# Kernel tuning notes

Measured on AMD Instinct MI355X. Metric: run time of the kernel, lower is better.

The kernel has to match this reference:

```python
import jax, jax.numpy as jnp
import numpy as np
from jax import lax

B, N, C_IN = 8, 4096, 64
NPOINT, NSAMPLE, RADIUS = 1024, 32, 0.2
BN_EPS = 1e-3  # keras BatchNormalization default epsilon


def _fps(pts):
    """Farthest point sampling on a single cloud pts: (N, 3) -> (NPOINT,) int32."""
    n = pts.shape[0]
    def step(carry, _):
        dist, far = carry
        c = pts[far]                                  # (3,)
        d = jnp.sum((pts - c) ** 2, axis=-1)          # (N,)
        dist = jnp.minimum(dist, d)
        nxt = jnp.argmax(dist).astype(jnp.int32)
        return (dist, nxt), far
    init = (jnp.full((n,), 1e10, pts.dtype), jnp.array(0, jnp.int32))
    _, idx = lax.scan(step, init, None, length=NPOINT)
    return idx


def _ball_query(xyz, new_xyz):
    """xyz: (B,N,3), new_xyz: (B,P,3) -> idx (B,P,NSAMPLE) int32.
    First NSAMPLE point indices within RADIUS of each centroid (in original
    order); slots beyond the in-ball count are filled with the first in-ball
    index, matching the PointNet++ CUDA query_ball_point semantics."""
    n = xyz.shape[1]
    # squared distances via the expansion trick to avoid a (B,P,N,3) temp
    d2 = (jnp.sum(new_xyz ** 2, -1)[:, :, None]
          + jnp.sum(xyz ** 2, -1)[:, None, :]
          - 2.0 * jnp.einsum('bpc,bnc->bpn', new_xyz, xyz))  # (B,P,N)
    in_ball = d2 < RADIUS ** 2
    cand = jnp.where(in_ball, jnp.arange(n, dtype=jnp.int32)[None, None, :], n)
    neg_top, _ = lax.top_k(-cand, NSAMPLE)   # NSAMPLE smallest indices
    idx = -neg_top                           # ascending order
    first = idx[..., :1]                     # centroid itself is always in-ball
    idx = jnp.where(idx == n, first, idx)
    return idx


def _group(feats, idx):
    """feats: (B,N,C), idx: (B,P,S) -> (B,P,S,C) gather per batch."""
    return jax.vmap(lambda f, i: f[i])(feats, idx)


def _mlp_layer(x, W, g, b, m, v):
    # 1x1 conv (no bias) + BN (inference stats) + ReLU
    x = jnp.einsum('bpsc,cd->bpsd', x, W)
    x = (x - m) * lax.rsqrt(v + BN_EPS) * g + b
    return jax.nn.relu(x)


def setup_inputs() -> dict:
    key = jax.random.key(0)
    ks = jax.random.split(key, 8)
    xyz = jax.random.uniform(ks[0], (B, N, 3), dtype=jnp.float32)
    points = jax.random.normal(ks[1], (B, N, C_IN), dtype=jnp.float32)
    c0 = 3 + C_IN  # use_xyz=True
    W0 = jax.random.normal(ks[2], (c0, 64), jnp.float32) / np.sqrt(c0)
    W1 = jax.random.normal(ks[3], (64, 64), jnp.float32) / np.sqrt(64.0)
    W2 = jax.random.normal(ks[4], (64, 128), jnp.float32) / np.sqrt(64.0)
    def bn(c):
        return (jnp.ones((c,), jnp.float32), jnp.zeros((c,), jnp.float32),
                jnp.zeros((c,), jnp.float32), jnp.ones((c,), jnp.float32))
    g0, b0, m0, v0 = bn(64)
    g1, b1, m1, v1 = bn(64)
    g2, b2, m2, v2 = bn(128)
    return dict(xyz=xyz, points=points,
                W0=W0, g0=g0, b0=b0, m0=m0, v0=v0,
                W1=W1, g1=g1, b1=b1, m1=m1, v1=v1,
                W2=W2, g2=g2, b2=b2, m2=m2, v2=v2)


def reference(xyz, points,
              W0, g0, b0, m0, v0,
              W1, g1, b1, m1, v1,
              W2, g2, b2, m2, v2):
    # --- sample_and_group ---
    fps_idx = jax.vmap(_fps)(xyz)                            # (B,P)
    new_xyz = jnp.take_along_axis(xyz, fps_idx[:, :, None], axis=1)  # (B,P,3)
    idx = _ball_query(xyz, new_xyz)                          # (B,P,S)
    grouped_xyz = _group(xyz, idx) - new_xyz[:, :, None, :]  # (B,P,S,3)
    grouped_pts = _group(points, idx)                        # (B,P,S,C)
    new_points = jnp.concatenate([grouped_xyz, grouped_pts], axis=-1)
    # --- shared per-point MLP (1x1 conv + BN + ReLU) ---
    new_points = _mlp_layer(new_points, W0, g0, b0, m0, v0)
    new_points = _mlp_layer(new_points, W1, g1, b1, m1, v1)
    new_points = _mlp_layer(new_points, W2, g2, b2, m2, v2)
    # --- max pool over the neighborhood axis ---
    new_points = jnp.max(new_points, axis=2)                 # (B,P,128)
    return new_xyz, new_points, idx
```

## Files before the change

kernel.cpp:

```cpp
#include <hip/hip_runtime.h>
#include <stdint.h>

#define BN_EPS 0.001f

typedef float v2f __attribute__((ext_vector_type(2)));


struct FpsSh {
  float px[4096], py[4096], pz[4096];
  unsigned long long wk[2][4];
  int curh[32];
};

struct WrkSh {
  float W0s[67 * 64];
  float W1s[64 * 64];
  float sh[64 * 36];
  float h0T[64 * 34];
  float s0c[64], t0c[64], s1c[64], t1c[64], s2c[128], t2c[128];
  float idxs[4 * 32];
  float cent[4 * 3];
};

union AllSh {
  FpsSh f;
  WrkSh w;
};

__global__ __launch_bounds__(256) void fused_kernel(
    const float* __restrict__ xyz, const float* __restrict__ points,
    const float* __restrict__ W0, const float* __restrict__ g0,
    const float* __restrict__ b0, const float* __restrict__ m0,
    const float* __restrict__ v0, const float* __restrict__ W1,
    const float* __restrict__ g1, const float* __restrict__ b1,
    const float* __restrict__ m1, const float* __restrict__ v1,
    const float* __restrict__ W2, const float* __restrict__ g2,
    const float* __restrict__ b2, const float* __restrict__ m2,
    const float* __restrict__ v2, float* __restrict__ new_xyz,
    float* __restrict__ new_points, float* __restrict__ idxf,
    unsigned int* __restrict__ prog) {
  __shared__ __align__(16) AllSh smem;
  const int bid = blockIdx.x;
  const int t = threadIdx.x;

  if (bid < 8) {
#pragma clang fp contract(off)
    float* px = smem.f.px;
    float* py = smem.f.py;
    float* pz = smem.f.pz;
    int* curh = smem.f.curh;
    auto& wk = smem.f.wk;
    const int lane = t & 63, wid = t >> 6;
    const int b = bid;
    const float* X = xyz + (size_t)b * 4096 * 3;
    float* out = new_xyz + (size_t)b * 1024 * 3;
    v2f x[8], y[8], z[8], dist[8];
#pragma unroll
    for (int j = 0; j < 8; ++j) {
      const int n0 = (2 * j) * 256 + t;
      const int n1 = (2 * j + 1) * 256 + t;
      x[j].x = X[n0 * 3 + 0]; x[j].y = X[n1 * 3 + 0];
      y[j].x = X[n0 * 3 + 1]; y[j].y = X[n1 * 3 + 1];
      z[j].x = X[n0 * 3 + 2]; z[j].y = X[n1 * 3 + 2];
      px[n0] = x[j].x; py[n0] = y[j].x; pz[n0] = z[j].x;
      px[n1] = x[j].y; py[n1] = y[j].y; pz[n1] = z[j].y;
      dist[j] = (v2f){1e10f, 1e10f};
    }
    __syncthreads();
    int cur = 0;
    for (int cc = 0; cc < 32; ++cc) {
      for (int ii = 0; ii < 32; ++ii) {
        const int it = cc * 32 + ii;
        if (t == 0) curh[ii] = cur;
        const float cx = px[cur], cy = py[cur], cz = pz[cur];
        const v2f cxv = {cx, cx}, cyv = {cy, cy}, czv = {cz, cz};
        float bestv = -1.0f;
        int bestj = 0;
#pragma unroll
        for (int j = 0; j < 8; ++j) {
          v2f dx = x[j] - cxv, dy = y[j] - cyv, dz = z[j] - czv;
          v2f d = dx * dx + dy * dy;
          d = d + dz * dz;
          v2f nd = __builtin_elementwise_min(dist[j], d);
          dist[j] = nd;
          if (nd.x > bestv) { bestv = nd.x; bestj = 2 * j; }
          if (nd.y > bestv) { bestv = nd.y; bestj = 2 * j + 1; }
        }
        const int besti = bestj * 256 + t;
        unsigned long long key =
            ((unsigned long long)__float_as_uint(bestv) << 32) | (unsigned)(~besti);
#define DPP_STEP(CTRL)                                                                     \
        {                                                                                  \
          unsigned lo_ = (unsigned)key, hi_ = (unsigned)(key >> 32);                       \
          unsigned ls = (unsigned)__builtin_amdgcn_update_dpp((int)lo_, (int)lo_, CTRL, 0xf, 0xf, false); \
          unsigned hs = (unsigned)__builtin_amdgcn_update_dpp((int)hi_, (int)hi_, CTRL, 0xf, 0xf, false); \
          unsigned long long sk = ((unsigned long long)hs << 32) | ls;                     \
          if (sk > key) key = sk;                                                          \
        }
        DPP_STEP(0x111)
        DPP_STEP(0x112)
        DPP_STEP(0x114)
        DPP_STEP(0x118)
        DPP_STEP(0x142)
        DPP_STEP(0x143)
#undef DPP_STEP
        const unsigned whi = (unsigned)__builtin_amdgcn_readlane((int)(key >> 32), 63);
        const unsigned wlo = (unsigned)__builtin_amdgcn_readlane((int)key, 63);
        if (lane == 0) wk[it & 1][wid] = ((unsigned long long)whi << 32) | wlo;
        __syncthreads();
        const unsigned long long k0 = wk[it & 1][0], k1 = wk[it & 1][1];
        const unsigned long long k2 = wk[it & 1][2], k3 = wk[it & 1][3];
        unsigned long long b01 = (k1 > k0) ? k1 : k0;
        unsigned long long b23 = (k3 > k2) ? k3 : k2;
        unsigned long long bk = (b23 > b01) ? b23 : b01;
        cur = (int)(~(unsigned)(bk & 0xffffffffull));
      }
      if (t == 0) {
        asm volatile("s_waitcnt vmcnt(0)" ::: "memory");
        if (cc > 0)
          __hip_atomic_store(&prog[b * 32], (unsigned)(cc * 32),
                             __ATOMIC_RELAXED, __HIP_MEMORY_SCOPE_AGENT);
      }
      if (t < 32) {
        const int c = curh[t];
        const int p = cc * 32 + t;
        __hip_atomic_store(&out[p * 3 + 0], px[c], __ATOMIC_RELAXED,
                           __HIP_MEMORY_SCOPE_AGENT);
        __hip_atomic_store(&out[p * 3 + 1], py[c], __ATOMIC_RELAXED,
                           __HIP_MEMORY_SCOPE_AGENT);
        __hip_atomic_store(&out[p * 3 + 2], pz[c], __ATOMIC_RELAXED,
                           __HIP_MEMORY_SCOPE_AGENT);
      }
      if (cc == 30 && t == 0) {
        asm volatile("s_waitcnt vmcnt(0)" ::: "memory");
        __hip_atomic_store(&prog[b * 32], 992u, __ATOMIC_RELAXED,
                           __HIP_MEMORY_SCOPE_AGENT);
      }
    }
    if (t == 0) {
      asm volatile("s_waitcnt vmcnt(0)" ::: "memory");
      __hip_atomic_store(&prog[b * 32], 1024u, __ATOMIC_RELAXED,
                         __HIP_MEMORY_SCOPE_AGENT);
    }
    return;
  }

  float* W0s = smem.w.W0s;
  float* W1s = smem.w.W1s;
  float* s0c = smem.w.s0c; float* t0c = smem.w.t0c;
  float* s1c = smem.w.s1c; float* t1c = smem.w.t1c;
  float* s2c = smem.w.s2c; float* t2c = smem.w.t2c;
  for (int i = t; i < 67 * 64; i += 256) W0s[i] = W0[i];
  for (int i = t; i < 64 * 64; i += 256) W1s[i] = W1[i];
  if (t < 64) {
    float s = g0[t] * rsqrtf(v0[t] + BN_EPS); s0c[t] = s; t0c[t] = b0[t] - m0[t] * s;
    float u = g1[t] * rsqrtf(v1[t] + BN_EPS); s1c[t] = u; t1c[t] = b1[t] - m1[t] * u;
  }
  if (t < 128) {
    float s = g2[t] * rsqrtf(v2[t] + BN_EPS); s2c[t] = s; t2c[t] = b2[t] - m2[t] * s;
  }
  __syncthreads();
  const int sgrp = t & 15, dgrp = t >> 4;
  const int dg2 = t & 31, sg2 = t >> 5;
  float* inT = smem.w.sh;
  float* h1T = smem.w.sh;
  float* h0T = smem.w.h0T;
  float* pmax = h0T;

  auto wait_prog = [&](int b, unsigned need) {
    int guard = 0;
    while (__hip_atomic_load(&prog[b * 32], __ATOMIC_RELAXED,
                             __HIP_MEMORY_SCOPE_AGENT) < need) {
      __builtin_amdgcn_s_sleep(8);
      if (++guard > (1 << 20)) break;
    }
  };

  auto process_group = [&](int b, int p0, int nc) {
    {
#pragma clang fp contract(off)
      const int wv = t >> 6, lane = t & 63;
      if (wv < nc) {
        const int pg = b * 1024 + p0 + wv;
        const float* X = xyz + (size_t)b * 4096 * 3;
        const float cx = __hip_atomic_load(&new_xyz[pg * 3 + 0], __ATOMIC_RELAXED,
                                           __HIP_MEMORY_SCOPE_AGENT);
        const float cy = __hip_atomic_load(&new_xyz[pg * 3 + 1], __ATOMIC_RELAXED,
                                           __HIP_MEMORY_SCOPE_AGENT);
        const float cz = __hip_atomic_load(&new_xyz[pg * 3 + 2], __ATOMIC_RELAXED,
                                           __HIP_MEMORY_SCOPE_AGENT);
        const float csq = (cx * cx + cy * cy) + cz * cz;
        float* outg = idxf + (size_t)pg * 32;
        float* ol = smem.w.idxs + wv * 32;
        int total = 0;
        int first = -1;
        float xx = X[lane * 3 + 0], yy = X[lane * 3 + 1], zz = X[lane * 3 + 2];
        for (int chunk = 0; chunk < 64; ++chunk) {
          const int n = chunk * 64 + lane;
          float nx = xx, ny = yy, nz = zz;
          if (chunk < 63) {
            const float* Xn = X + (n + 64) * 3;
            nx = Xn[0]; ny = Xn[1]; nz = Xn[2];
          }
          const float sq = (xx * xx + yy * yy) + zz * zz;
          const float dot = fmaf(cz, zz, fmaf(cy, yy, cx * xx));
          const float d2 = (csq + sq) - 2.0f * dot;
          const bool in = d2 < 0.04f;
          const unsigned long long mask = __ballot(in);
          if (first < 0 && mask != 0ull) first = chunk * 64 + __builtin_ctzll(mask);
          if (in) {
            const int pos = total + __builtin_popcountll(mask & ((1ull << lane) - 1ull));
            if (pos < 32) { outg[pos] = (float)n; ol[pos] = (float)n; }
          }
          total += __builtin_popcountll(mask);
          if (total >= 32) break;
          xx = nx; yy = ny; zz = nz;
        }
        if (total < 32 && first >= 0) {
          const int slot = total + lane;
          if (slot < 32) { outg[slot] = (float)first; ol[slot] = (float)first; }
        }
        if (lane == 0) {
          smem.w.cent[wv * 3 + 0] = cx;
          smem.w.cent[wv * 3 + 1] = cy;
          smem.w.cent[wv * 3 + 2] = cz;
        }
      }
    }
    __syncthreads();
    for (int pp = 0; pp < nc; ++pp) {
      const int pg = b * 1024 + p0 + pp;
      const float cx = smem.w.cent[pp * 3 + 0];
      const float cy = smem.w.cent[pp * 3 + 1];
      const float cz = smem.w.cent[pp * 3 + 2];
      {
        const int s = t >> 3, cg = t & 7;
        const int i = (int)smem.w.idxs[pp * 32 + s];
        const float* Pr = points + ((size_t)b * 4096 + i) * 64 + cg * 8;
        const float4 a = *(const float4*)Pr;
        const float4 c4 = *(const float4*)(Pr + 4);
        const int r = 3 + cg * 8;
        inT[(r + 0) * 34 + s] = a.x;  inT[(r + 1) * 34 + s] = a.y;
        inT[(r + 2) * 34 + s] = a.z;  inT[(r + 3) * 34 + s] = a.w;
        inT[(r + 4) * 34 + s] = c4.x; inT[(r + 5) * 34 + s] = c4.y;
        inT[(r + 6) * 34 + s] = c4.z; inT[(r + 7) * 34 + s] = c4.w;
        if (t < 32) {
          const int i2 = (int)smem.w.idxs[pp * 32 + t];
          const float* Xr = xyz + ((size_t)b * 4096 + i2) * 3;
          inT[0 * 34 + t] = Xr[0] - cx;
          inT[1 * 34 + t] = Xr[1] - cy;
          inT[2 * 34 + t] = Xr[2] - cz;
        }
      }
      __syncthreads();
      {
        float acc[2][4] = {{0, 0, 0, 0}, {0, 0, 0, 0}};
#pragma unroll 4
        for (int c = 0; c < 67; ++c) {
          const float2 a = *(const float2*)&inT[c * 34 + 2 * sgrp];
          const float4 w = *(const float4*)&W0s[c * 64 + 4 * dgrp];
          acc[0][0] = fmaf(a.x, w.x, acc[0][0]); acc[0][1] = fmaf(a.x, w.y, acc[0][1]);
          acc[0][2] = fmaf(a.x, w.z, acc[0][2]); acc[0][3] = fmaf(a.x, w.w, acc[0][3]);
          acc[1][0] = fmaf(a.y, w.x, acc[1][0]); acc[1][1] = fmaf(a.y, w.y, acc[1][1]);
          acc[1][2] = fmaf(a.y, w.z, acc[1][2]); acc[1][3] = fmaf(a.y, w.w, acc[1][3]);
        }
#pragma unroll
        for (int dj = 0; dj < 4; ++dj) {
          const int d = 4 * dgrp + dj;
          const float s = s0c[d], bb = t0c[d];
#pragma unroll
          for (int si = 0; si < 2; ++si) {
            float yv = fmaf(acc[si][dj], s, bb);
            h0T[d * 34 + 2 * sgrp + si] = fmaxf(yv, 0.0f);
          }
        }
      }
      __syncthreads();
      {
        float acc[2][4] = {{0, 0, 0, 0}, {0, 0, 0, 0}};
#pragma unroll 4
        for (int c = 0; c < 64; ++c) {
          const float2 a = *(const float2*)&h0T[c * 34 + 2 * sgrp];
          const float4 w = *(const float4*)&W1s[c * 64 + 4 * dgrp];
          acc[0][0] = fmaf(a.x, w.x, acc[0][0]); acc[0][1] = fmaf(a.x, w.y, acc[0][1]);
          acc[0][2] = fmaf(a.x, w.z, acc[0][2]); acc[0][3] = fmaf(a.x, w.w, acc[0][3]);
          acc[1][0] = fmaf(a.y, w.x, acc[1][0]); acc[1][1] = fmaf(a.y, w.y, acc[1][1]);
          acc[1][2] = fmaf(a.y, w.z, acc[1][2]); acc[1][3] = fmaf(a.y, w.w, acc[1][3]);
        }
#pragma unroll
        for (int dj = 0; dj < 4; ++dj) {
          const int d = 4 * dgrp + dj;
          const float s = s1c[d], bb = t1c[d];
#pragma unroll
          for (int si = 0; si < 2; ++si) {
            float yv = fmaf(acc[si][dj], s, bb);
            h1T[d * 36 + 2 * sgrp + si] = fmaxf(yv, 0.0f);
          }
        }
      }
      __syncthreads();
      {
        float acc[4][4] = {{0,0,0,0},{0,0,0,0},{0,0,0,0},{0,0,0,0}};
#pragma unroll 8
        for (int c = 0; c < 64; ++c) {
          const float4 a = *(const float4*)&h1T[c * 36 + 4 * sg2];
          const float4 w = *(const float4*)(W2 + c * 128 + 4 * dg2);
          acc[0][0] = fmaf(a.x, w.x, acc[0][0]); acc[0][1] = fmaf(a.x, w.y, acc[0][1]);
          acc[0][2] = fmaf(a.x, w.z, acc[0][2]); acc[0][3] = fmaf(a.x, w.w, acc[0][3]);
          acc[1][0] = fmaf(a.y, w.x, acc[1][0]); acc[1][1] = fmaf(a.y, w.y, acc[1][1]);
          acc[1][2] = fmaf(a.y, w.z, acc[1][2]); acc[1][3] = fmaf(a.y, w.w, acc[1][3]);
          acc[2][0] = fmaf(a.z, w.x, acc[2][0]); acc[2][1] = fmaf(a.z, w.y, acc[2][1]);
          acc[2][2] = fmaf(a.z, w.z, acc[2][2]); acc[2][3] = fmaf(a.z, w.w, acc[2][3]);
          acc[3][0] = fmaf(a.w, w.x, acc[3][0]); acc[3][1] = fmaf(a.w, w.y, acc[3][1]);
          acc[3][2] = fmaf(a.w, w.z, acc[3][2]); acc[3][3] = fmaf(a.w, w.w, acc[3][3]);
        }
#pragma unroll
        for (int dj = 0; dj < 4; ++dj) {
          const int d = 4 * dg2 + dj;
          const float s = s2c[d], bb = t2c[d];
          float mx = 0.0f;
#pragma unroll
          for (int si = 0; si < 4; ++si) {
            float yv = fmaf(acc[si][dj], s, bb);
            mx = fmaxf(mx, fmaxf(yv, 0.0f));
          }
          pmax[sg2 * 128 + d] = mx;
        }
      }
      __syncthreads();
      if (t < 128) {
        float mx = pmax[t];
#pragma unroll
        for (int g = 1; g < 8; ++g) mx = fmaxf(mx, pmax[g * 128 + t]);
        new_points[(size_t)pg * 128 + t] = mx;
      }
      __syncthreads();
    }
  };

  if (bid >= 256) {
    const int sid = bid - 256;
    const int b = sid & 7;
    const int q = sid >> 3;
    wait_prog(b, (unsigned)(960 + q + 1));
    process_group(b, 960 + q, 1);
    wait_prog(b, (unsigned)(992 + q + 1));
    process_group(b, 992 + q, 1);
  } else {
    for (int k = bid - 8; k < 1920; k += 248) {
      const int j = k >> 3, b = k & 7;
      wait_prog(b, (unsigned)(j * 4 + 4));
      process_group(b, j * 4, 4);
    }
  }
}

extern "C" void kernel_launch(void* const* d_in, const int* in_sizes, int n_in,
                              void* d_out, int out_size, void* d_ws, size_t ws_size,
                              hipStream_t stream) {
  (void)in_sizes; (void)n_in; (void)out_size; (void)ws_size;
  const float* xyz    = (const float*)d_in[0];
  const float* points = (const float*)d_in[1];
  const float* W0 = (const float*)d_in[2];
  const float* g0 = (const float*)d_in[3];
  const float* b0 = (const float*)d_in[4];
  const float* m0 = (const float*)d_in[5];
  const float* v0 = (const float*)d_in[6];
  const float* W1 = (const float*)d_in[7];
  const float* g1 = (const float*)d_in[8];
  const float* b1 = (const float*)d_in[9];
  const float* m1 = (const float*)d_in[10];
  const float* v1 = (const float*)d_in[11];
  const float* W2 = (const float*)d_in[12];
  const float* g2 = (const float*)d_in[13];
  const float* b2 = (const float*)d_in[14];
  const float* m2 = (const float*)d_in[15];
  const float* v2 = (const float*)d_in[16];

  float* new_xyz    = (float*)d_out;
  float* new_points = new_xyz + 8 * 1024 * 3;
  float* idxf       = new_points + 8 * 1024 * 128;

  unsigned int* prog = (unsigned int*)d_ws;
  hipMemsetAsync(d_ws, 0, 8 * 32 * sizeof(unsigned int), stream);
  fused_kernel<<<512, 256, 0, stream>>>(xyz, points, W0, g0, b0, m0, v0,
                                        W1, g1, b1, m1, v1,
                                        W2, g2, b2, m2, v2,
                                        new_xyz, new_points, idxf, prog);
}
```

Before: 699.8 us.

## Split FPS and worker shared memory, adaptive spin sleep, rebalance tail groups

The FPS and worker shared-memory layouts now sit in two separate arrays instead of one union, so every block reserves both (about 49KB plus 41KB). This lowers the number of blocks that fit per CU. The spin-wait sleeps longer when the producer is far behind, to cut polling traffic while FPS runs. Points 960-991 move from the single-point tail blocks into the 4-point group loop, so tail blocks only handle the last 32 points. This changes how consumers overlap with the sequential FPS producer but may reduce occupancy.

Measured after the change: 709.3 us. No clear change (+1.3%).

```diff
diff --git a/kernel.cpp b/kernel.cpp
--- a/kernel.cpp
+++ b/kernel.cpp
@@ -20,11 +20,6 @@
   float s0c[64], t0c[64], s1c[64], t1c[64], s2c[128], t2c[128];
   float idxs[4 * 32];
   float cent[4 * 3];
-};
-
-union AllSh {
-  FpsSh f;
-  WrkSh w;
 };
 
 __global__ __launch_bounds__(256) void fused_kernel(
@@ -39,17 +34,18 @@
     const float* __restrict__ v2, float* __restrict__ new_xyz,
     float* __restrict__ new_points, float* __restrict__ idxf,
     unsigned int* __restrict__ prog) {
-  __shared__ __align__(16) AllSh smem;
+  __shared__ __align__(16) FpsSh smemF;
+  __shared__ __align__(16) WrkSh smemW;
   const int bid = blockIdx.x;
   const int t = threadIdx.x;
 
   if (bid < 8) {
 #pragma clang fp contract(off)
-    float* px = smem.f.px;
-    float* py = smem.f.py;
-    float* pz = smem.f.pz;
-    int* curh = smem.f.curh;
-    auto& wk = smem.f.wk;
+    float* px = smemF.px;
+    float* py = smemF.py;
+    float* pz = smemF.pz;
+    int* curh = smemF.curh;
+    auto& wk = smemF.wk;
     const int lane = t & 63, wid = t >> 6;
     const int b = bid;
     const float* X = xyz + (size_t)b * 4096 * 3;
@@ -145,11 +141,11 @@
     return;
   }
 
-  float* W0s = smem.w.W0s;
-  float* W1s = smem.w.W1s;
-  float* s0c = smem.w.s0c; float* t0c = smem.w.t0c;
-  float* s1c = smem.w.s1c; float* t1c = smem.w.t1c;
-  float* s2c = smem.w.s2c; float* t2c = smem.w.t2c;
+  float* W0s = smemW.W0s;
+  float* W1s = smemW.W1s;
+  float* s0c = smemW.s0c; float* t0c = smemW.t0c;
+  float* s1c = smemW.s1c; float* t1c = smemW.t1c;
+  float* s2c = smemW.s2c; float* t2c = smemW.t2c;
   for (int i = t; i < 67 * 64; i += 256) W0s[i] = W0[i];
   for (int i = t; i < 64 * 64; i += 256) W1s[i] = W1[i];
   if (t < 64) {
@@ -162,16 +158,22 @@
   __syncthreads();
   const int sgrp = t & 15, dgrp = t >> 4;
   const int dg2 = t & 31, sg2 = t >> 5;
-  float* inT = smem.w.sh;
-  float* h1T = smem.w.sh;
-  float* h0T = smem.w.h0T;
+  float* inT = smemW.sh;
+  float* h1T = smemW.sh;
+  float* h0T = smemW.h0T;
   float* pmax = h0T;
 
   auto wait_prog = [&](int b, unsigned need) {
     int guard = 0;
-    while (__hip_atomic_load(&prog[b * 32], __ATOMIC_RELAXED,
-                             __HIP_MEMORY_SCOPE_AGENT) < need) {
-      __builtin_amdgcn_s_sleep(8);
+    for (;;) {
+      const unsigned p = __hip_atomic_load(&prog[b * 32], __ATOMIC_RELAXED,
+                                           __HIP_MEMORY_SCOPE_AGENT);
+      if (p >= need) break;
+      if (need - p > 32) {
+        __builtin_amdgcn_s_sleep(64);
+      } else {
+        __builtin_amdgcn_s_sleep(8);
+      }
       if (++guard > (1 << 20)) break;
     }
   };
@@ -191,7 +193,7 @@
                                            __HIP_MEMORY_SCOPE_AGENT);
         const float csq = (cx * cx + cy * cy) + cz * cz;
         float* outg = idxf + (size_t)pg * 32;
-        float* ol = smem.w.idxs + wv * 32;
+        float* ol = smemW.idxs + wv * 32;
         int total = 0;
         int first = -1;
         float xx = X[lane * 3 + 0], yy = X[lane * 3 + 1], zz = X[lane * 3 + 2];
@@ -221,21 +223,21 @@
           if (slot < 32) { outg[slot] = (float)first; ol[slot] = (float)first; }
         }
         if (lane == 0) {
-          smem.w.cent[wv * 3 + 0] = cx;
-          smem.w.cent[wv * 3 + 1] = cy;
-          smem.w.cent[wv * 3 + 2] = cz;
+          smemW.cent[wv * 3 + 0] = cx;
+          smemW.cent[wv * 3 + 1] = cy;
+          smemW.cent[wv * 3 + 2] = cz;
         }
       }
     }
     __syncthreads();
     for (int pp = 0; pp < nc; ++pp) {
       const int pg = b * 1024 + p0 + pp;
-      const float cx = smem.w.cent[pp * 3 + 0];
-      const float cy = smem.w.cent[pp * 3 + 1];
-      const float cz = smem.w.cent[pp * 3 + 2];
+      const float cx = smemW.cent[pp * 3 + 0];
+      const float cy = smemW.cent[pp * 3 + 1];
+      const float cz = smemW.cent[pp * 3 + 2];
       {
         const int s = t >> 3, cg = t & 7;
-        const int i = (int)smem.w.idxs[pp * 32 + s];
+        const int i = (int)smemW.idxs[pp * 32 + s];
         const float* Pr = points + ((size_t)b * 4096 + i) * 64 + cg * 8;
         const float4 a = *(const float4*)Pr;
         const float4 c4 = *(const float4*)(Pr + 4);
@@ -245,7 +247,7 @@
         inT[(r + 4) * 34 + s] = c4.x; inT[(r + 5) * 34 + s] = c4.y;
         inT[(r + 6) * 34 + s] = c4.z; inT[(r + 7) * 34 + s] = c4.w;
         if (t < 32) {
-          const int i2 = (int)smem.w.idxs[pp * 32 + t];
+          const int i2 = (int)smemW.idxs[pp * 32 + t];
           const float* Xr = xyz + ((size_t)b * 4096 + i2) * 3;
           inT[0 * 34 + t] = Xr[0] - cx;
           inT[1 * 34 + t] = Xr[1] - cy;
@@ -342,12 +344,10 @@
     const int sid = bid - 256;
     const int b = sid & 7;
     const int q = sid >> 3;
-    wait_prog(b, (unsigned)(960 + q + 1));
-    process_group(b, 960 + q, 1);
     wait_prog(b, (unsigned)(992 + q + 1));
     process_group(b, 992 + q, 1);
   } else {
-    for (int k = bid - 8; k < 1920; k += 248) {
+    for (int k = bid - 8; k < 1984; k += 248) {
       const int j = k >> 3, b = k & 7;
       wait_prog(b, (unsigned)(j * 4 + 4));
       process_group(b, j * 4, 4);
@@ -382,7 +382,7 @@
   float* idxf       = new_points + 8 * 1024 * 128;
 
   unsigned int* prog = (unsigned int*)d_ws;
-  hipMemsetAsync(d_ws, 0, 8 * 32 * sizeof(unsigned int), stream);
+  (void)hipMemsetAsync(d_ws, 0, 8 * 32 * sizeof(unsigned int), stream);
   fused_kernel<<<512, 256, 0, stream>>>(xyz, points, W0, g0, b0, m0, v0,
                                         W1, g1, b1, m1, v1,
                                         W2, g2, b2, m2, v2,
```
